# Kernel tuning notes

Measured on AMD Instinct MI355X. Metric: run time of the kernel, lower is better.

## Reference

```python
import jax, jax.numpy as jnp
import numpy as np

B_IMG, T_PER, DIN = 8, 4096, 1176
D, E, BN, L, TOP_K, OUT = 1024, 8, 64, 4, 2, 4096


def setup_inputs() -> dict:
    key = jax.random.key(0)
    ks = jax.random.split(key, 16)
    s = 0.02
    inp = {
        "pixel_values": jax.random.normal(ks[0], (B_IMG * T_PER, DIN), jnp.float32),
        "image_grid_thw": jnp.tile(jnp.array([[1, 64, 64]], dtype=jnp.int64), (B_IMG, 1)),
        # in_proj (no bias)
        "w_in": jax.random.normal(ks[1], (DIN, D), jnp.float32) * s,
        # skin classifier: Linear(D,64) -> ReLU -> Linear(64,3)
        "w_sc1": jax.random.normal(ks[2], (D, 64), jnp.float32) * s,
        "b_sc1": jnp.zeros((64,), jnp.float32),
        "w_sc2": jax.random.normal(ks[3], (64, 3), jnp.float32) * s,
        "b_sc2": jnp.zeros((3,), jnp.float32),
        # per-adapter-layer routers (stacked over L)
        "w_rimg": jax.random.normal(ks[4], (L, D, E), jnp.float32) * s,
        "w_rskin": jax.random.normal(ks[5], (L, 3, E), jnp.float32) * s,
        # per-layer, per-expert MLP: Linear(D,BN) -> ReLU -> Linear(BN,D)
        "ew1": jax.random.normal(ks[6], (L, E, D, BN), jnp.float32) * s,
        "eb1": jnp.zeros((L, E, BN), jnp.float32),
        "ew2": jax.random.normal(ks[7], (L, E, BN, D), jnp.float32) * s,
        "eb2": jnp.zeros((L, E, D), jnp.float32),
        # out_proj
        "w_out": jax.random.normal(ks[8], (D, OUT), jnp.float32) * s,
        "b_out": jnp.zeros((OUT,), jnp.float32),
    }
    return inp


def _forward(pixel_values, image_grid_thw, w_in, w_sc1, b_sc1, w_sc2, b_sc2,
             w_rimg, w_rskin, ew1, eb1, ew2, eb2, w_out, b_out):
    B = image_grid_thw.shape[0]
    T = pixel_values.shape[0] // B  # equal chunk sizes (t*h*w identical per image)
    x = pixel_values.reshape(B, T, -1)

    def per_image(xc):  # xc: [T, din]
        h = xc @ w_in  # [T, D]
        g = h.mean(0)
        skin_logits = jax.nn.relu(g @ w_sc1 + b_sc1) @ w_sc2 + b_sc2  # [3]
        skin_probs = jax.nn.softmax(skin_logits)

        def layer(carry, params):
            h, aux = carry
            wri, wrs, W1, B1, W2, B2 = params
            logits = h @ wri + skin_probs @ wrs  # [T, E]
            probs = jax.nn.softmax(logits, axis=-1)
            tp, ti = jax.lax.top_k(probs, TOP_K)
            tp = tp / (tp.sum(-1, keepdims=True) + 1e-6)
            rows = jnp.arange(h.shape[0])[:, None]
            # dense per-token expert weights (0 for non-selected experts)
            wfull = jnp.zeros_like(probs).at[rows, ti].add(tp)
            mask = jnp.zeros_like(probs).at[rows, ti].add(1.0)
            h1 = jax.nn.relu(jnp.einsum('td,edb->teb', h, W1) + B1)  # [T,E,BN]
            h2 = jnp.einsum('teb,ebd->ted', h1, W2) + B2             # [T,E,D]
            moe_out = jnp.einsum('ted,te->td', h2, wfull)
            aux = aux + (probs.mean(0) * mask.mean(0)).sum() * probs.shape[-1]
            return (h + moe_out, aux), None

        (h, aux), _ = jax.lax.scan(layer, (h, jnp.zeros((), h.dtype)),
                                   (w_rimg, w_rskin, ew1, eb1, ew2, eb2))
        return h.mean(0), skin_logits, aux

    pooled, skin_logits, aux = jax.vmap(per_image)(x)
    vision_proj = pooled @ w_out + b_out
    return pooled, vision_proj, aux.sum(), skin_logits


def reference(pixel_values, image_grid_thw, w_in, w_sc1, b_sc1, w_sc2, b_sc2,
              w_rimg, w_rskin, ew1, eb1, ew2, eb2, w_out, b_out):
    return _forward(pixel_values, image_grid_thw, w_in, w_sc1, b_sc1, w_sc2, b_sc2,
                    w_rimg, w_rskin, ew1, eb1, ew2, eb2, w_out, b_out)
```

## Files before the change

### kernel.cpp

```cpp
#include <hip/hip_runtime.h>
#include <math.h>

#define TPI  4096
#define TT   32768
#define DIN  1176
#define KP   1216
#define DM   1024
#define NE   8
#define BN   64
#define NL   4
#define DOUT 4096

typedef __attribute__((ext_vector_type(4))) float floatx4;
typedef __attribute__((ext_vector_type(8))) short bf16x8;
typedef unsigned int uint;

__device__ inline short f2bf(float x) {
    unsigned u = __float_as_uint(x);
    u += 0x7fffu + ((u >> 16) & 1u);
    return (short)(u >> 16);
}
__device__ inline float bf2f(short h) {
    return __uint_as_float(((unsigned)(unsigned short)h) << 16);
}

#define GLP(p) ((const __attribute__((address_space(1))) void*)(p))
#define LDSP(p) ((__attribute__((address_space(3))) void*)(p))
#define ASYNC16(g, s) __builtin_amdgcn_global_load_lds(GLP(g), LDSP(s), 16, 0, 0)

#define OFF_H0    0ul
#define OFF_H1    67108864ul
#define OFF_XB    67108864ul
#define OFF_WBT   146800640ul
#define OFF_E1T   149291008ul
#define OFF_E2T   153485312ul
#define OFF_BTOK  157679616ul
#define OFF_BW1   157810688ul
#define OFF_BW2   157941760ul
#define OFF_T2E   158072832ul
#define OFF_T2W   158203904ul
#define OFF_Z     158466048ul
#define Z_BYTES   39232ul
#define OFF_RB    158505280ul
#define OFF_WRT   158506304ul

__global__ __launch_bounds__(256) void convx_kernel(
    const float* __restrict__ X, short* __restrict__ Xb)
{
    const long row = blockIdx.x;
    const float* src = X + row * (long)DIN;
    short* dst = Xb + row * (long)KP;
    for (int i = threadIdx.x; i < 304; i += 256) {
        short4 s;
        if (i < 294) {
            float4 v = *(const float4*)(src + i * 4);
            s.x = f2bf(v.x); s.y = f2bf(v.y); s.z = f2bf(v.z); s.w = f2bf(v.w);
        } else {
            s.x = 0; s.y = 0; s.z = 0; s.w = 0;
        }
        *(short4*)(dst + i * 4) = s;
    }
}

__global__ __launch_bounds__(256) void transp_kernel(
    const float* __restrict__ src, short* __restrict__ dst, int RS, int CS, int DK)
{
    __shared__ float tb[64][65];
    const int kt = blockIdx.x * 64, nt = blockIdx.y * 64;
    const long sb = (long)blockIdx.z * RS * CS;
    const long db = (long)blockIdx.z * CS * DK;
    const int rr = threadIdx.x >> 6, cc = threadIdx.x & 63;
#pragma unroll
    for (int i = 0; i < 16; ++i) {
        int r = i * 4 + rr;
        int k = kt + r, n = nt + cc;
        tb[r][cc] = (k < RS && n < CS) ? src[sb + (long)k * CS + n] : 0.0f;
    }
    __syncthreads();
#pragma unroll
    for (int i = 0; i < 16; ++i) {
        int r = i * 4 + rr;
        int n = nt + r, k = kt + cc;
        if (n < CS && k < DK) dst[db + (long)n * DK + k] = f2bf(tb[cc][r]);
    }
}

__global__ __launch_bounds__(256) void wrt_kernel(
    const float* __restrict__ w_rimg, short* __restrict__ wrT)
{
    const int l = blockIdx.x >> 4, e = blockIdx.x & 15;
    short* dst = wrT + ((long)l * 16 + e) * 1024;
    if (e < 8) {
        const float* src = w_rimg + (long)l * 8192 + e;
        for (int k = threadIdx.x; k < 1024; k += 256) dst[k] = f2bf(src[k * 8]);
    } else {
        for (int k = threadIdx.x; k < 1024; k += 256) dst[k] = 0;
    }
}
// ... 7 lines not shown
    const int tid = threadIdx.x;
    const int m0 = blockIdx.x * 128, n0 = blockIdx.y * 128;
    const int w = tid >> 6, lane = tid & 63;
    const int quad = lane >> 4, l15 = lane & 15;
    const int wm = (w >> 1) * 64, wn = (w & 1) * 64;

    floatx4 acc[4][4];
#pragma unroll
    for (int i = 0; i < 4; ++i)
#pragma unroll
        for (int j = 0; j < 4; ++j) acc[i][j] = 0.0f;

    const int r = tid >> 3;
    const int gofs = ((tid & 7) ^ (r & 7)) * 8;
    const short* ap = Xb + (long)(m0 + r) * KP + gofs;
    const short* bp = Wbt + (long)(n0 + r) * KP + gofs;
    short* asd = As + tid * 8;
    short* bsd = Bs + tid * 8;
    const int rx = l15 & 7;

    for (int k0 = 0; k0 < KP; k0 += 64) {
        __syncthreads();
#pragma unroll
        for (int i = 0; i < 4; ++i) {
            ASYNC16(ap + (long)i * 32 * KP + k0, asd + i * 2048);
            ASYNC16(bp + (long)i * 32 * KP + k0, bsd + i * 2048);
        }
        __syncthreads();
#pragma unroll
        for (int kk = 0; kk < 2; ++kk) {
            bf16x8 af[4], bfr[4];
#pragma unroll
            for (int i = 0; i < 4; ++i)
                af[i] = *(const bf16x8*)&As[(wm + i * 16 + l15) * 64 + (((kk * 4 + quad)) ^ rx) * 8];
#pragma unroll
            for (int j = 0; j < 4; ++j)
                bfr[j] = *(const bf16x8*)&Bs[(wn + j * 16 + l15) * 64 + (((kk * 4 + quad)) ^ rx) * 8];
#pragma unroll
            for (int i = 0; i < 4; ++i)
#pragma unroll
                for (int j = 0; j < 4; ++j)
                    acc[i][j] = __builtin_amdgcn_mfma_f32_16x16x32_bf16(af[i], bfr[j], acc[i][j], 0, 0, 0);
        }
    }
    const int img = m0 >> 12;
#pragma unroll
    for (int j = 0; j < 4; ++j) {
        float cs = 0.0f;
#pragma unroll
        for (int i = 0; i < 4; ++i)
#pragma unroll
            for (int r2 = 0; r2 < 4; ++r2) {
                short hv = f2bf(acc[i][j][r2]);
                Hb[(long)(m0 + wm + i * 16 + quad * 4 + r2) * DM + n0 + wn + j * 16 + l15] = hv;
                cs += bf2f(hv);
            }
        cs += __shfl_xor(cs, 16);
        cs += __shfl_xor(cs, 32);
        if (quad == 0)
            atomicAdd(&g[img * DM + n0 + wn + j * 16 + l15], cs * (1.0f / 4096.0f));
    }
}

__global__ __launch_bounds__(256) void colmean_kernel(
    const short* __restrict__ Hb, float* __restrict__ outp)
{
    const int col = blockIdx.x * 256 + threadIdx.x;
    const int img = blockIdx.y;
    const int t0 = blockIdx.z * 256;
    const short* p = Hb + ((long)img * TPI + t0) * DM + col;
    float s = 0.0f;
#pragma unroll 8
    for (int t = 0; t < 256; ++t) s += bf2f(p[(long)t * DM]);
    atomicAdd(&outp[img * DM + col], s * (1.0f / 4096.0f));
}

__global__ __launch_bounds__(256) void skin1_kernel(
    const float* __restrict__ g, const float* __restrict__ w_sc1,
    const float* __restrict__ b_sc1, float* __restrict__ hsg)
{
    __shared__ float red[4][64];
    const int img = blockIdx.x;
    const int part = threadIdx.x >> 6, c = threadIdx.x & 63;
    float s = 0.0f;
    for (int i = 0; i < 256; ++i) {
        int d = part * 256 + i;
        s += g[img * DM + d] * w_sc1[d * 64 + c];
    }
    red[part][c] = s;
    __syncthreads();
    if (part == 0) {
        float v = red[0][c] + red[1][c] + red[2][c] + red[3][c] + b_sc1[c];
        hsg[img * 64 + c] = fmaxf(v, 0.0f);
    }
}

__global__ __launch_bounds__(256) void skin2_kernel(
    const float* __restrict__ hsg, const float* __restrict__ w_sc2, const float* __restrict__ b_sc2,
    const float* __restrict__ w_rskin, float* __restrict__ skin_logits_out, float* __restrict__ rb)
{
    __shared__ float l3[24];
    __shared__ float sp[24];
    const int tid = threadIdx.x;
    if (tid < 24) {
        int img = tid / 3, j = tid % 3;
        float s = b_sc2[j];
        for (int c = 0; c < 64; ++c) s += hsg[img * 64 + c] * w_sc2[c * 3 + j];
// ... 95 lines not shown
        }
#pragma unroll
        for (int e = 0; e < 8; ++e) {
            float rsum = p[e];
            for (int off = 32; off > 0; off >>= 1) rsum += __shfl_down(rsum, off);
            if (tid == 0) atomicAdd(&sum_probs[l * 64 + img * 8 + e], rsum);
        }
    }
}

__global__ __launch_bounds__(256) void scatter_kernel(
    const uint* __restrict__ top2e, const float* __restrict__ top2w,
    const int* __restrict__ counts_pair, int* __restrict__ cursors,
    int* __restrict__ btok, float* __restrict__ bw1, float* __restrict__ bw2, int l)
{
    __shared__ int pofS[64];
    const int tid = threadIdx.x;
    if (tid < 64) {
        int c = counts_pair[l * 64 + tid];
        int x = c;
#pragma unroll
        for (int off = 1; off < 64; off <<= 1) {
            int y = __shfl_up(x, off);
            if (tid >= off) x += y;
        }
        pofS[tid] = x - c;
    }
    __syncthreads();
    const int t = blockIdx.x * 256 + tid;
    const int lane = tid & 63;
    uint pe = top2e[t];
    int p = (int)(pe & 255u) * 8 + (int)((pe >> 8) & 255u);
    float w1 = top2w[2 * t], w2 = top2w[2 * t + 1];
    int myoff = pofS[p];
    unsigned long long rem = __ballot(true);
    while (rem) {
        int leader = __ffsll(rem) - 1;
        int pv = __shfl(p, leader);
        unsigned long long m = __ballot(p == pv);
        int basep = 0;
        if (lane == leader) basep = atomicAdd(&cursors[l * 64 + pv], __popcll(m));
        basep = __shfl(basep, leader);
        if (p == pv) {
            int pos = basep + __popcll(m & ((1ull << lane) - 1ull));
            int s = myoff + pos;
            btok[s] = t;
            bw1[s] = w1;
            bw2[s] = w2;
        }
        rem &= ~m;
    }
}

__global__ __launch_bounds__(256) void expert_pair(
    const short* __restrict__ Hin, short* __restrict__ Hout,
    int* __restrict__ counts_pair,
    const int* __restrict__ btok, const float* __restrict__ bw1, const float* __restrict__ bw2,
    const short* __restrict__ ew1t, const float* __restrict__ eb1,
    const short* __restrict__ ew2t, const float* __restrict__ eb2,
    const short* __restrict__ wrT, const float* __restrict__ rb,
    uint* __restrict__ top2e, float* __restrict__ top2w,
    float* __restrict__ sum_probs, float* __restrict__ mask_cnt, int l)
{
    __shared__ __align__(16) short As[8 * 64 * 32];
    __shared__ __align__(16) short h1a[64 * 72];
    __shared__ __align__(16) short h1b[64 * 72];
    __shared__ int tkS[64];
    __shared__ float w1S[64], w2S[64];
    __shared__ int pofS[64], cntS[64], tpS[64];
    __shared__ int nworkS;
    __shared__ float spLDS[64], mkLDS[64];

    const int tid = threadIdx.x;
    const int w = tid >> 6, lane = tid & 63;
    const int quad = lane >> 4, l15 = lane & 15;
    short* sdst = As + tid * 8;

    if (tid < 64) {
        int c = counts_pair[l * 64 + tid];
        cntS[tid] = c;
        int x = c;
#pragma unroll
        for (int off = 1; off < 64; off <<= 1) {
            int y = __shfl_up(x, off);
            if (tid >= off) x += y;
        }
        pofS[tid] = x - c;
        int nb = (c + 63) >> 6;
        int t = nb;
#pragma unroll
        for (int off = 1; off < 64; off <<= 1) {
            int y = __shfl_up(t, off);
            if (tid >= off) t += y;
        }
        tpS[tid] = t;
        if (tid == 63) nworkS = t;
    }
    __syncthreads();
    const int nwork = nworkS;

    for (int wi = blockIdx.x; wi < nwork; wi += gridDim.x) {
        int p = 0;
        while (p < 63 && tpS[p] <= wi) ++p;
        const int cnt = cntS[p];
        const int nbp = (cnt + 63) >> 6;
        const int base = (wi - (tpS[p] - nbp)) * 64;
        const int ea = p >> 3, eb = p & 7;
        const int off = pofS[p];

        __syncthreads();
        if (tid < 64) {
            bool valid = (base + tid) < cnt;
            int s = off + base + tid;
            tkS[tid] = valid ? btok[s] : 0;
            w1S[tid] = valid ? bw1[s] : 0.0f;
            w2S[tid] = valid ? bw2[s] : 0.0f;
            spLDS[tid] = 0.0f;
            mkLDS[tid] = 0.0f;
        }
        __syncthreads();
        const int lea = l * 8 + ea, leb = l * 8 + eb;
        const short* rowptr = Hin + (long)tkS[w * 16 + (lane >> 2)] * DM + (lane & 3) * 8;

        floatx4 acc1a[4], acc1b[4];
#pragma unroll
        for (int i = 0; i < 4; ++i) { acc1a[i] = 0.0f; acc1b[i] = 0.0f; }
        const short* w1ap = ew1t + ((long)lea * 64 + w * 16 + l15) * DM + quad * 8;
        const short* w1bp = ew1t + ((long)leb * 64 + w * 16 + l15) * DM + quad * 8;

        for (int k0 = 0; k0 < DM; k0 += 256) {
            __syncthreads();
#pragma unroll
            for (int c = 0; c < 8; ++c) ASYNC16(rowptr + k0 + c * 32, sdst + c * 2048);
            __syncthreads();
#pragma unroll
            for (int c = 0; c < 8; ++c) {
                bf16x8 ba = *(const bf16x8*)(w1ap + k0 + c * 32);
                bf16x8 bb = *(const bf16x8*)(w1bp + k0 + c * 32);
#pragma unroll
                for (int i = 0; i < 4; ++i) {
                    bf16x8 af = *(const bf16x8*)&As[c * 2048 + (i * 16 + l15) * 32 + quad * 8];
                    acc1a[i] = __builtin_amdgcn_mfma_f32_16x16x32_bf16(af, ba, acc1a[i], 0, 0, 0);
                    acc1b[i] = __builtin_amdgcn_mfma_f32_16x16x32_bf16(af, bb, acc1b[i], 0, 0, 0);
                }
            }
        }
        {
            float b1av = eb1[lea * BN + w * 16 + l15];
            float b1bv = eb1[leb * BN + w * 16 + l15];
#pragma unroll
            for (int i = 0; i < 4; ++i)
#pragma unroll
                for (int r = 0; r < 4; ++r) {
                    h1a[(i * 16 + quad * 4 + r) * 72 + w * 16 + l15] =
                        f2bf(fmaxf(acc1a[i][r] + b1av, 0.0f));
                    h1b[(i * 16 + quad * 4 + r) * 72 + w * 16 + l15] =
                        f2bf(fmaxf(acc1b[i][r] + b1bv, 0.0f));
                }
        }
        __syncthreads();

        const short* w2ap = ew2t + ((long)lea * DM + w * 16 + l15) * 64 + quad * 8;
        const short* w2bp = ew2t + ((long)leb * DM + w * 16 + l15) * 64 + quad * 8;
        const bool rowvalid = (base + (tid >> 2)) < cnt;
        const long orow = (long)tkS[tid >> 2] * DM;

        floatx4 acc_lg[4];
#pragma unroll
        for (int tf = 0; tf < 4; ++tf) acc_lg[tf] = 0.0f;

        for (int gidx = 0; gidx < 4; ++gidx) {
            const int g0 = gidx * 256;
#pragma unroll
            for (int c = 0; c < 8; ++c) ASYNC16(rowptr + g0 + c * 32, sdst + c * 2048);
            __syncthreads();
#pragma unroll
            for (int ns = 0; ns < 4; ++ns) {
                const int n0 = g0 + ns * 64;
                floatx4 a2a[4], a2b[4];
#pragma unroll
                for (int tj = 0; tj < 4; ++tj) { a2a[tj] = 0.0f; a2b[tj] = 0.0f; }
#pragma unroll
                for (int kk = 0; kk < 2; ++kk) {
                    bf16x8 wa = *(const bf16x8*)(w2ap + (long)n0 * 64 + kk * 32);
                    bf16x8 wb = *(const bf16x8*)(w2bp + (long)n0 * 64 + kk * 32);
#pragma unroll
                    for (int tj = 0; tj < 4; ++tj) {
                        bf16x8 ha = *(const bf16x8*)&h1a[(tj * 16 + l15) * 72 + kk * 32 + quad * 8];
                        bf16x8 hb = *(const bf16x8*)&h1b[(tj * 16 + l15) * 72 + kk * 32 + quad * 8];
                        a2a[tj] = __builtin_amdgcn_mfma_f32_16x16x32_bf16(wa, ha, a2a[tj], 0, 0, 0);
                        a2b[tj] = __builtin_amdgcn_mfma_f32_16x16x32_bf16(wb, hb, a2b[tj], 0, 0, 0);
                    }
                }
                const int nloc = ns * 64 + w * 16 + quad * 4;
                const int csub = nloc >> 5, cidx = nloc & 31;
                float4 b2av = *(const float4*)&eb2[lea * DM + g0 + nloc];
                float4 b2bv = *(const float4*)&eb2[leb * DM + g0 + nloc];
#pragma unroll
                for (int tj = 0; tj < 4; ++tj) {
                    int tk = tj * 16 + l15;
                    float w1 = w1S[tk], w2 = w2S[tk];
                    short* slot = &As[csub * 2048 + tk * 32 + cidx];
                    short4 res = *(short4*)slot;
                    short4 o;
                    o.x = f2bf(bf2f(res.x) + w1 * (a2a[tj][0] + b2av.x) + w2 * (a2b[tj][0] + b2bv.x));
                    o.y = f2bf(bf2f(res.y) + w1 * (a2a[tj][1] + b2av.y) + w2 * (a2b[tj][1] + b2bv.y));
                    o.z = f2bf(bf2f(res.z) + w1 * (a2a[tj][2] + b2av.z) + w2 * (a2b[tj][2] + b2bv.z));
                    o.w = f2bf(bf2f(res.w) + w1 * (a2a[tj][3] + b2av.w) + w2 * (a2b[tj][3] + b2bv.w));
                    *(short4*)slot = o;
                }
            }
            __syncthreads();

            if (l < 3) {
                const short* wrp = wrT + ((long)(l + 1) * 16 + l15) * 1024 + g0 + w * 64 + quad * 8;
#pragma unroll
                for (int kk = 0; kk < 2; ++kk) {
                    bf16x8 wf = *(const bf16x8*)(wrp + kk * 32);
#pragma unroll
                    for (int tf = 0; tf < 4; ++tf) {
                        bf16x8 of = *(const bf16x8*)&As[(w * 2 + kk) * 2048 + (tf * 16 + l15) * 32 + quad * 8];
                        acc_lg[tf] = __builtin_amdgcn_mfma_f32_16x16x32_bf16(wf, of, acc_lg[tf], 0, 0, 0);
                    }
                }
            }
            if (rowvalid) {
                const int tok = tid >> 2;
#pragma unroll
                for (int c2 = 0; c2 < 2; ++c2) {
                    const int csub = (tid & 3) * 2 + c2;
#pragma unroll
                    for (int j = 0; j < 4; ++j) {
                        int4 v = *(const int4*)&As[csub * 2048 + tok * 32 + j * 8];
                        *(int4*)(Hout + orow + g0 + csub * 32 + j * 8) = v;
                    }
                }
            }
            __syncthreads();
        }

        if (l < 3) {
            float* lgF = (float*)As;
#pragma unroll
            for (int tf = 0; tf < 4; ++tf)
                *(floatx4*)&lgF[(w * 64 + tf * 16 + l15) * 16 + quad * 4] = acc_lg[tf];
            __syncthreads();
            if (tid < 64) {
                const bool valid = (base + tid) < cnt;
                const int token = tkS[tid];
                const int img = token >> 12;
                float pb[8]; float mx = -1e30f;
#pragma unroll
                for (int e = 0; e < 8; ++e) {
                    float v = lgF[tid * 16 + e] + lgF[(64 + tid) * 16 + e]
                            + lgF[(128 + tid) * 16 + e] + lgF[(192 + tid) * 16 + e]
                            + rb[(l + 1) * 64 + img * 8 + e];
                    pb[e] = v; mx = fmaxf(mx, v);
                }
                float s = 0.0f;
#pragma unroll
                for (int e = 0; e < 8; ++e) { pb[e] = expf(pb[e] - mx); s += pb[e]; }
                float inv = 1.0f / s;
#pragma unroll
                for (int e = 0; e < 8; ++e) pb[e] *= inv;
                int i1 = 0; float b1v = pb[0];
#pragma unroll
                for (int e = 1; e < 8; ++e) if (pb[e] > b1v) { b1v = pb[e]; i1 = e; }
                int i2 = -1; float b2v = -1.0f;
#pragma unroll
                for (int e = 0; e < 8; ++e) if (e != i1 && pb[e] > b2v) { b2v = pb[e]; i2 = e; }
                if (valid) {
                    float den = b1v + b2v + 1e-6f;
                    top2e[token] = (uint)i1 | ((uint)i2 << 8);
                    top2w[2 * token] = b1v / den;
                    top2w[2 * token + 1] = b2v / den;
                    atomicAdd(&counts_pair[(l + 1) * 64 + i1 * 8 + i2], 1);
#pragma unroll
                    for (int e = 0; e < 8; ++e) atomicAdd(&spLDS[img * 8 + e], pb[e]);
                    atomicAdd(&mkLDS[img * 8 + i1], 1.0f);
                    atomicAdd(&mkLDS[img * 8 + i2], 1.0f);
                }
            }
            __syncthreads();
            if (tid < 64) {
                float v = spLDS[tid];
                if (v != 0.0f) atomicAdd(&sum_probs[(l + 1) * 64 + tid], v);
                float mz = mkLDS[tid];
                if (mz != 0.0f) atomicAdd(&mask_cnt[(l + 1) * 64 + tid], mz);
            }
        }
    }
}

__global__ __launch_bounds__(256) void vproj_kernel(
    const float* __restrict__ pooled, const float* __restrict__ w_out,
    const float* __restrict__ b_out, float* __restrict__ outp)
{
    __shared__ float ps[8 * 128];
    const int tid = threadIdx.x;
    const int n = blockIdx.x * 256 + tid;
    const int d0 = blockIdx.y * 128;
#pragma unroll
    for (int i = 0; i < 4; ++i) {
        int idx = tid + i * 256;
        ps[idx] = pooled[(idx >> 7) * DM + d0 + (idx & 127)];
    }
    __syncthreads();
    float acc[8];
    float binit = (blockIdx.y == 0) ? b_out[n] : 0.0f;
#pragma unroll
    for (int img = 0; img < 8; ++img) acc[img] = binit;
    for (int d = 0; d < 128; ++d) {
        float wv = w_out[(long)(d0 + d) * DOUT + n];
#pragma unroll
        for (int img = 0; img < 8; ++img) acc[img] += ps[img * 128 + d] * wv;
    }
#pragma unroll
    for (int img = 0; img < 8; ++img) atomicAdd(&outp[img * DOUT + n], acc[img]);
}

__global__ __launch_bounds__(64) void aux_kernel(
    const float* __restrict__ sum_probs, const float* __restrict__ mask_cnt,
    float* __restrict__ outp)
{
    const int tid = threadIdx.x;
    float v = 0.0f;
    if (tid < 32) {
        float s = 0.0f;
#pragma unroll
        for (int e = 0; e < 8; ++e) s += sum_probs[tid * 8 + e] * mask_cnt[tid * 8 + e];
        v = s * (8.0f / (4096.0f * 4096.0f));
    }
    for (int off = 32; off > 0; off >>= 1) v += __shfl_down(v, off);
    if (tid == 0) outp[0] = v;
}

extern "C" void kernel_launch(void* const* d_in, const int* in_sizes, int n_in,
                              void* d_out, int out_size, void* d_ws, size_t ws_size,
                              hipStream_t stream) {
    const float* X       = (const float*)d_in[0];
    const float* w_in    = (const float*)d_in[2];
    const float* w_sc1   = (const float*)d_in[3];
    const float* b_sc1   = (const float*)d_in[4];
    const float* w_sc2   = (const float*)d_in[5];
    const float* b_sc2   = (const float*)d_in[6];
    const float* w_rimg  = (const float*)d_in[7];
    const float* w_rskin = (const float*)d_in[8];
    const float* ew1     = (const float*)d_in[9];
    const float* eb1     = (const float*)d_in[10];
    const float* ew2     = (const float*)d_in[11];
    const float* eb2     = (const float*)d_in[12];
    const float* w_out   = (const float*)d_in[13];
    const float* b_out   = (const float*)d_in[14];

    float* out = (float*)d_out;
    char* ws = (char*)d_ws;

    short* H0   = (short*)(ws + OFF_H0);
    short* H1   = (short*)(ws + OFF_H1);
    short* Xb   = (short*)(ws + OFF_XB);
    short* Wbt  = (short*)(ws + OFF_WBT);
    short* ew1t = (short*)(ws + OFF_E1T);
    short* ew2t = (short*)(ws + OFF_E2T);
    int*   btok = (int*)(ws + OFF_BTOK);
    float* bw1  = (float*)(ws + OFF_BW1);
    float* bw2  = (float*)(ws + OFF_BW2);
    uint*  top2e = (uint*)(ws + OFF_T2E);
    float* top2w = (float*)(ws + OFF_T2W);
    int*   counts_pair = (int*)(ws + OFF_Z);
    int*   cursors     = (int*)(ws + OFF_Z + 1024);
    float* sum_probs   = (float*)(ws + OFF_Z + 2368);
    float* mask_cnt    = (float*)(ws + OFF_Z + 3392);
    float* g           = (float*)(ws + OFF_Z + 4416);
    float* hsg         = (float*)(ws + OFF_Z + 37184);
    float* rb          = (float*)(ws + OFF_RB);
    short* wrT         = (short*)(ws + OFF_WRT);

    hipMemsetAsync(d_out, 0, (size_t)out_size * sizeof(float), stream);
    hipMemsetAsync(ws + OFF_Z, 0, Z_BYTES, stream);

    dim3 b256(256);
    convx_kernel<<<TT, b256, 0, stream>>>(X, Xb);
    transp_kernel<<<dim3(19, 16, 1), b256, 0, stream>>>(w_in, Wbt, DIN, DM, KP);
    transp_kernel<<<dim3(16, 1, 32), b256, 0, stream>>>(ew1, ew1t, DM, BN, DM);
    transp_kernel<<<dim3(1, 16, 32), b256, 0, stream>>>(ew2, ew2t, BN, DM, BN);
    wrt_kernel<<<64, b256, 0, stream>>>(w_rimg, wrT);
    gemm_in_mfma<<<dim3(256, 8), b256, 0, stream>>>(Xb, Wbt, H0, g);
    skin1_kernel<<<8, b256, 0, stream>>>(g, w_sc1, b_sc1, hsg);
    skin2_kernel<<<1, b256, 0, stream>>>(hsg, w_sc2, b_sc2, w_rskin, out + 40961, rb);
    router_kernel<<<512, b256, 0, stream>>>(H0, wrT, rb, top2e, top2w,
                                            counts_pair, sum_probs, mask_cnt, 0);

    short* Hc = H0;
    short* Hn = H1;
    for (int l = 0; l < NL; ++l) {
        scatter_kernel<<<128, b256, 0, stream>>>(top2e, top2w, counts_pair, cursors,
                                                 btok, bw1, bw2, l);
        expert_pair<<<576, b256, 0, stream>>>(Hc, Hn, counts_pair, btok, bw1, bw2,
                                              ew1t, eb1, ew2t, eb2, wrT, rb,
                                              top2e, top2w, sum_probs, mask_cnt, l);
        short* tmp = Hc; Hc = Hn; Hn = tmp;
    }
    colmean_kernel<<<dim3(4, 8, 16), b256, 0, stream>>>(Hc, out);
    vproj_kernel<<<dim3(16, 8), b256, 0, stream>>>(out, w_out, b_out, out + 8192);
    aux_kernel<<<1, 64, 0, stream>>>(sum_probs, mask_cnt, out + 40960);
}
```

Measured before the change: 1.419 ms.

## Stage full 64-token hidden tile in LDS once per expert-pair work item

Measured after the change: 1.557 ms. 1.1x slower.

```diff
diff --git a/kernel.cpp b/kernel.cpp
--- a/kernel.cpp
+++ b/kernel.cpp
@@ -44,6 +44,21 @@
 #define OFF_RB    158505280ul
 #define OFF_WRT   158506304ul
 
+#define EPS_XS    0
+#define EPS_H1A   131072
+#define EPS_H1B   140288
+#define EPS_LGF   131072
+#define EPS_TK    149504
+#define EPS_W1    149760
+#define EPS_W2    150016
+#define EPS_CNT   150272
+#define EPS_POF   150528
+#define EPS_TP    150784
+#define EPS_SP    151040
+#define EPS_MK    151296
+#define EPS_NW    151552
+#define EP_SMEM   151616
+
 __global__ __launch_bounds__(256) void convx_kernel(
     const float* __restrict__ X, short* __restrict__ Xb)
 {
@@ -157,7 +172,8 @@
 #pragma unroll
             for (int r2 = 0; r2 < 4; ++r2) {
                 short hv = f2bf(acc[i][j][r2]);
-                Hb[(long)(m0 + wm + i * 16 + quad * 4 + r2) * DM + n0 + wn + j * 16 + l15] = hv;
+                Hb[(long)(m0 + wm + i * 16 + quad * 4 + r2) * DM + n0 + wn + j * 16 + l15] =
+                    hv;
                 cs += bf2f(hv);
             }
         cs += __shfl_xor(cs, 16);
@@ -359,7 +375,7 @@
     }
 }
 
-__global__ __launch_bounds__(256) void expert_pair(
+__global__ __launch_bounds__(256, 1) void expert_pair(
     const short* __restrict__ Hin, short* __restrict__ Hout,
     int* __restrict__ counts_pair,
     const int* __restrict__ btok, const float* __restrict__ bw1, const float* __restrict__ bw2,
@@ -369,19 +385,25 @@
     uint* __restrict__ top2e, float* __restrict__ top2w,
     float* __restrict__ sum_probs, float* __restrict__ mask_cnt, int l)
 {
-    __shared__ __align__(16) short As[8 * 64 * 32];
-    __shared__ __align__(16) short h1a[64 * 72];
-    __shared__ __align__(16) short h1b[64 * 72];
-    __shared__ int tkS[64];
-    __shared__ float w1S[64], w2S[64];
-    __shared__ int pofS[64], cntS[64], tpS[64];
-    __shared__ int nworkS;
-    __shared__ float spLDS[64], mkLDS[64];
+    extern __shared__ __align__(16) char smem[];
+    short* Xs   = (short*)(smem + EPS_XS);
+    short* h1a  = (short*)(smem + EPS_H1A);
+    short* h1b  = (short*)(smem + EPS_H1B);
+    float* lgF  = (float*)(smem + EPS_LGF);
+    int*   tkS  = (int*)(smem + EPS_TK);
+    float* w1S  = (float*)(smem + EPS_W1);
+    float* w2S  = (float*)(smem + EPS_W2);
+    int*   cntS = (int*)(smem + EPS_CNT);
+    int*   pofS = (int*)(smem + EPS_POF);
+    int*   tpS  = (int*)(smem + EPS_TP);
+    float* spLDS = (float*)(smem + EPS_SP);
+    float* mkLDS = (float*)(smem + EPS_MK);
+    int*   nworkS = (int*)(smem + EPS_NW);
 
     const int tid = threadIdx.x;
     const int w = tid >> 6, lane = tid & 63;
     const int quad = lane >> 4, l15 = lane & 15;
-    short* sdst = As + tid * 8;
+    const int rx = l15 & 7;
 
     if (tid < 64) {
         int c = counts_pair[l * 64 + tid];
@@ -401,10 +423,10 @@
             if (tid >= off) t += y;
         }
         tpS[tid] = t;
-        if (tid == 63) nworkS = t;
+        if (tid == 63) nworkS[0] = t;
     }
     __syncthreads();
-    const int nwork = nworkS;
+    const int nwork = nworkS[0];
 
     for (int wi = blockIdx.x; wi < nwork; wi += gridDim.x) {
         int p = 0;
@@ -414,6 +436,7 @@
         const int base = (wi - (tpS[p] - nbp)) * 64;
         const int ea = p >> 3, eb = p & 7;
         const int off = pofS[p];
+        const int lea = l * 8 + ea, leb = l * 8 + eb;
 
         __syncthreads();
         if (tid < 64) {
@@ -426,30 +449,35 @@
             mkLDS[tid] = 0.0f;
         }
         __syncthreads();
-        const int lea = l * 8 + ea, leb = l * 8 + eb;
-        const short* rowptr = Hin + (long)tkS[w * 16 + (lane >> 2)] * DM + (lane & 3) * 8;
-
-        floatx4 acc1a[4], acc1b[4];
-#pragma unroll
-        for (int i = 0; i < 4; ++i) { acc1a[i] = 0.0f; acc1b[i] = 0.0f; }
+
+        {
+            const int hb = tid >> 7;
+            const int lch = tid & 127;
+#pragma unroll
+            for (int i = 0; i < 32; ++i) {
+                const int row = i * 2 + hb;
+                const int tok = tkS[row];
+                const short* src = Hin + (long)tok * DM + ((lch ^ (row & 7)) << 3);
+                ASYNC16(src, Xs + (i * 256 + tid) * 8);
+            }
+        }
         const short* w1ap = ew1t + ((long)lea * 64 + w * 16 + l15) * DM + quad * 8;
         const short* w1bp = ew1t + ((long)leb * 64 + w * 16 + l15) * DM + quad * 8;
-
-        for (int k0 = 0; k0 < DM; k0 += 256) {
-            __syncthreads();
-#pragma unroll
-            for (int c = 0; c < 8; ++c) ASYNC16(rowptr + k0 + c * 32, sdst + c * 2048);
-            __syncthreads();
-#pragma unroll
-            for (int c = 0; c < 8; ++c) {
-                bf16x8 ba = *(const bf16x8*)(w1ap + k0 + c * 32);
-                bf16x8 bb = *(const bf16x8*)(w1bp + k0 + c * 32);
-#pragma unroll
-                for (int i = 0; i < 4; ++i) {
-                    bf16x8 af = *(const bf16x8*)&As[c * 2048 + (i * 16 + l15) * 32 + quad * 8];
-                    acc1a[i] = __builtin_amdgcn_mfma_f32_16x16x32_bf16(af, ba, acc1a[i], 0, 0, 0);
-                    acc1b[i] = __builtin_amdgcn_mfma_f32_16x16x32_bf16(af, bb, acc1b[i], 0, 0, 0);
-                }
+        __syncthreads();
+
+        floatx4 acc1a[4], acc1b[4];
+#pragma unroll
+        for (int i = 0; i < 4; ++i) { acc1a[i] = 0.0f; acc1b[i] = 0.0f; }
+#pragma unroll 8
+        for (int ks = 0; ks < 32; ++ks) {
+            bf16x8 ba = *(const bf16x8*)(w1ap + ks * 32);
+            bf16x8 bb = *(const bf16x8*)(w1bp + ks * 32);
+            const int cpos = ((ks * 4 + quad) ^ rx) * 8;
+#pragma unroll
+            for (int i = 0; i < 4; ++i) {
+                bf16x8 af = *(const bf16x8*)&Xs[(i * 16 + l15) * 1024 + cpos];
+                acc1a[i] = __builtin_amdgcn_mfma_f32_16x16x32_bf16(af, ba, acc1a[i], 0, 0, 0);
+                acc1b[i] = __builtin_amdgcn_mfma_f32_16x16x32_bf16(af, bb, acc1b[i], 0, 0, 0);
             }
         }
         {
@@ -467,87 +495,85 @@
         }
         __syncthreads();
 
+        bf16x8 hra[2][4], hrb[2][4];
+#pragma unroll
+        for (int kk = 0; kk < 2; ++kk)
+#pragma unroll
+            for (int tj = 0; tj < 4; ++tj) {
+                hra[kk][tj] = *(const bf16x8*)&h1a[(tj * 16 + l15) * 72 + kk * 32 + quad * 8];
+                hrb[kk][tj] = *(const bf16x8*)&h1b[(tj * 16 + l15) * 72 + kk * 32 + quad * 8];
+            }
+
         const short* w2ap = ew2t + ((long)lea * DM + w * 16 + l15) * 64 + quad * 8;
         const short* w2bp = ew2t + ((long)leb * DM + w * 16 + l15) * 64 + quad * 8;
-        const bool rowvalid = (base + (tid >> 2)) < cnt;
-        const long orow = (long)tkS[tid >> 2] * DM;
-
-        floatx4 acc_lg[4];
-#pragma unroll
-        for (int tf = 0; tf < 4; ++tf) acc_lg[tf] = 0.0f;
-
-        for (int gidx = 0; gidx < 4; ++gidx) {
-            const int g0 = gidx * 256;
-#pragma unroll
-            for (int c = 0; c < 8; ++c) ASYNC16(rowptr + g0 + c * 32, sdst + c * 2048);
-            __syncthreads();
-#pragma unroll
-            for (int ns = 0; ns < 4; ++ns) {
-                const int n0 = g0 + ns * 64;
-                floatx4 a2a[4], a2b[4];
-#pragma unroll
-                for (int tj = 0; tj < 4; ++tj) { a2a[tj] = 0.0f; a2b[tj] = 0.0f; }
-#pragma unroll
-                for (int kk = 0; kk < 2; ++kk) {
-                    bf16x8 wa = *(const bf16x8*)(w2ap + (long)n0 * 64 + kk * 32);
-                    bf16x8 wb = *(const bf16x8*)(w2bp + (long)n0 * 64 + kk * 32);
-#pragma unroll
-                    for (int tj = 0; tj < 4; ++tj) {
-                        bf16x8 ha = *(const bf16x8*)&h1a[(tj * 16 + l15) * 72 + kk * 32 + quad * 8];
-                        bf16x8 hb = *(const bf16x8*)&h1b[(tj * 16 + l15) * 72 + kk * 32 + quad * 8];
-                        a2a[tj] = __builtin_amdgcn_mfma_f32_16x16x32_bf16(wa, ha, a2a[tj], 0, 0, 0);
-                        a2b[tj] = __builtin_amdgcn_mfma_f32_16x16x32_bf16(wb, hb, a2b[tj], 0, 0, 0);
-                    }
+        const int nl = w * 16 + quad * 4;
+
+        for (int sl = 0; sl < 16; ++sl) {
+            const int n0 = sl * 64;
+            floatx4 a2a[4], a2b[4];
+#pragma unroll
+            for (int tj = 0; tj < 4; ++tj) { a2a[tj] = 0.0f; a2b[tj] = 0.0f; }
+#pragma unroll
+            for (int kk = 0; kk < 2; ++kk) {
+                bf16x8 wa = *(const bf16x8*)(w2ap + (long)n0 * 64 + kk * 32);
+                bf16x8 wb = *(const bf16x8*)(w2bp + (long)n0 * 64 + kk * 32);
+#pragma unroll
+                for (int tj = 0; tj < 4; ++tj) {
+                    a2a[tj] = __builtin_amdgcn_mfma_f32_16x16x32_bf16(wa, hra[kk][tj], a2a[tj], 0, 0, 0);
+                    a2b[tj] = __builtin_amdgcn_mfma_f32_16x16x32_bf16(wb, hrb[kk][tj], a2b[tj], 0, 0, 0);
                 }
-                const int nloc = ns * 64 + w * 16 + quad * 4;
-                const int csub = nloc >> 5, cidx = nloc & 31;
-                float4 b2av = *(const float4*)&eb2[lea * DM + g0 + nloc];
-                float4 b2bv = *(const float4*)&eb2[leb * DM + g0 + nloc];
-#pragma unroll
-                for (int tj = 0; tj < 4; ++tj) {
-                    int tk = tj * 16 + l15;
-                    float w1 = w1S[tk], w2 = w2S[tk];
-                    short* slot = &As[csub * 2048 + tk * 32 + cidx];
-                    short4 res = *(short4*)slot;
-                    short4 o;
-                    o.x = f2bf(bf2f(res.x) + w1 * (a2a[tj][0] + b2av.x) + w2 * (a2b[tj][0] + b2bv.x));
-                    o.y = f2bf(bf2f(res.y) + w1 * (a2a[tj][1] + b2av.y) + w2 * (a2b[tj][1] + b2bv.y));
-                    o.z = f2bf(bf2f(res.z) + w1 * (a2a[tj][2] + b2av.z) + w2 * (a2b[tj][2] + b2bv.z));
-                    o.w = f2bf(bf2f(res.w) + w1 * (a2a[tj][3] + b2av.w) + w2 * (a2b[tj][3] + b2bv.w));
-                    *(short4*)slot = o;
+            }
+            const int gcol = n0 + nl;
+            const int cpos2 = ((gcol >> 3) ^ rx) * 8 + (gcol & 7);
+            float4 b2av = *(const float4*)&eb2[lea * DM + gcol];
+            float4 b2bv = *(const float4*)&eb2[leb * DM + gcol];
+#pragma unroll
+            for (int tj = 0; tj < 4; ++tj) {
+                int tk = tj * 16 + l15;
+                float w1v = w1S[tk], w2v = w2S[tk];
+                short* slot = &Xs[tk * 1024 + cpos2];
+                short4 res = *(short4*)slot;
+                short4 o;
+                o.x = f2bf(bf2f(res.x) + w1v * (a2a[tj][0] + b2av.x) + w2v * (a2b[tj][0] + b2bv.x));
+                o.y = f2bf(bf2f(res.y) + w1v * (a2a[tj][1] + b2av.y) + w2v * (a2b[tj][1] + b2bv.y));
+                o.z = f2bf(bf2f(res.z) + w1v * (a2a[tj][2] + b2av.z) + w2v * (a2b[tj][2] + b2bv.z));
+                o.w = f2bf(bf2f(res.w) + w1v * (a2a[tj][3] + b2av.w) + w2v * (a2b[tj][3] + b2bv.w));
+                *(short4*)slot = o;
+            }
+        }
+        __syncthreads();
+
+        {
+            const int orowi = tid >> 2;
+            const bool rowvalid = (base + orowi) < cnt;
+            if (rowvalid) {
+                const long orow = (long)tkS[orowi] * DM;
+                const int k = orowi & 7;
+#pragma unroll
+                for (int i = 0; i < 32; ++i) {
+                    const int ch = (tid & 3) + i * 4;
+                    int4 v = *(const int4*)&Xs[orowi * 1024 + ((ch ^ k) << 3)];
+                    *(int4*)(Hout + orow + (ch << 3)) = v;
                 }
             }
-            __syncthreads();
-
-            if (l < 3) {
-                const short* wrp = wrT + ((long)(l + 1) * 16 + l15) * 1024 + g0 + w * 64 + quad * 8;
-#pragma unroll
-                for (int kk = 0; kk < 2; ++kk) {
-                    bf16x8 wf = *(const bf16x8*)(wrp + kk * 32);
-#pragma unroll
-                    for (int tf = 0; tf < 4; ++tf) {
-                        bf16x8 of = *(const bf16x8*)&As[(w * 2 + kk) * 2048 + (tf * 16 + l15) * 32 + quad * 8];
-                        acc_lg[tf] = __builtin_amdgcn_mfma_f32_16x16x32_bf16(wf, of, acc_lg[tf], 0, 0, 0);
-                    }
+        }
+
+        if (l < 3) {
+            const short* wrp = wrT + ((long)(l + 1) * 16 + l15) * 1024 + quad * 8;
+            floatx4 acc_lg[4];
+#pragma unroll
+            for (int tf = 0; tf < 4; ++tf) acc_lg[tf] = 0.0f;
+#pragma unroll
+            for (int kl = 0; kl < 8; ++kl) {
+                const int ks = w * 8 + kl;
+                bf16x8 wf = *(const bf16x8*)(wrp + ks * 32);
+                const int cpos = ((ks * 4 + quad) ^ rx) * 8;
+#pragma unroll
+                for (int tf = 0; tf < 4; ++tf) {
+                    bf16x8 of = *(const bf16x8*)&Xs[(tf * 16 + l15) * 1024 + cpos];
+                    acc_lg[tf] = __builtin_amdgcn_mfma_f32_16x16x32_bf16(wf, of, acc_lg[tf], 0, 0, 0);
                 }
             }
-            if (rowvalid) {
-                const int tok = tid >> 2;
-#pragma unroll
-                for (int c2 = 0; c2 < 2; ++c2) {
-                    const int csub = (tid & 3) * 2 + c2;
-#pragma unroll
-                    for (int j = 0; j < 4; ++j) {
-                        int4 v = *(const int4*)&As[csub * 2048 + tok * 32 + j * 8];
-                        *(int4*)(Hout + orow + g0 + csub * 32 + j * 8) = v;
-                    }
-                }
-            }
-            __syncthreads();
-        }
-
-        if (l < 3) {
-            float* lgF = (float*)As;
 #pragma unroll
             for (int tf = 0; tf < 4; ++tf)
                 *(floatx4*)&lgF[(w * 64 + tf * 16 + l15) * 16 + quad * 4] = acc_lg[tf];
@@ -683,6 +709,13 @@
     float* rb          = (float*)(ws + OFF_RB);
     short* wrT         = (short*)(ws + OFF_WRT);
 
+    static bool attr_set = false;
+    if (!attr_set) {
+        hipFuncSetAttribute(reinterpret_cast<const void*>(expert_pair),
+                            hipFuncAttributeMaxDynamicSharedMemorySize, EP_SMEM);
+        attr_set = true;
+    }
+
     hipMemsetAsync(d_out, 0, (size_t)out_size * sizeof(float), stream);
     hipMemsetAsync(ws + OFF_Z, 0, Z_BYTES, stream);
 
@@ -703,9 +736,9 @@
     for (int l = 0; l < NL; ++l) {
         scatter_kernel<<<128, b256, 0, stream>>>(top2e, top2w, counts_pair, cursors,
                                                  btok, bw1, bw2, l);
-        expert_pair<<<576, b256, 0, stream>>>(Hc, Hn, counts_pair, btok, bw1, bw2,
-                                              ew1t, eb1, ew2t, eb2, wrT, rb,
-                                              top2e, top2w, sum_probs, mask_cnt, l);
+        expert_pair<<<576, b256, EP_SMEM, stream>>>(Hc, Hn, counts_pair, btok, bw1, bw2,
+                                                    ew1t, eb1, ew2t, eb2, wrT, rb,
+                                                    top2e, top2w, sum_probs, mask_cnt, l);
         short* tmp = Hc; Hc = Hn; Hn = tmp;
     }
     colmean_kernel<<<dim3(4, 8, 16), b256, 0, stream>>>(Hc, out);
```

## Restructure expert_pair into independent per-wave 16-token tiles without block barriers

Applied to the files above, without the earlier changes.

Measured after the change: 4.626 ms. 226% more time.

```diff
diff --git a/kernel.cpp b/kernel.cpp
--- a/kernel.cpp
+++ b/kernel.cpp
@@ -157,7 +157,8 @@
 #pragma unroll
             for (int r2 = 0; r2 < 4; ++r2) {
                 short hv = f2bf(acc[i][j][r2]);
-                Hb[(long)(m0 + wm + i * 16 + quad * 4 + r2) * DM + n0 + wn + j * 16 + l15] = hv;
+                Hb[(long)(m0 + wm + i * 16 + quad * 4 + r2) * DM + n0 + wn + j * 16 + l15] =
+                    hv;
                 cs += bf2f(hv);
             }
         cs += __shfl_xor(cs, 16);
@@ -359,7 +360,7 @@
     }
 }
 
-__global__ __launch_bounds__(256) void expert_pair(
+__global__ __launch_bounds__(256, 2) void expert_pair(
     const short* __restrict__ Hin, short* __restrict__ Hout,
     int* __restrict__ counts_pair,
     const int* __restrict__ btok, const float* __restrict__ bw1, const float* __restrict__ bw2,
@@ -369,231 +370,177 @@
     uint* __restrict__ top2e, float* __restrict__ top2w,
     float* __restrict__ sum_probs, float* __restrict__ mask_cnt, int l)
 {
-    __shared__ __align__(16) short As[8 * 64 * 32];
-    __shared__ __align__(16) short h1a[64 * 72];
-    __shared__ __align__(16) short h1b[64 * 72];
-    __shared__ int tkS[64];
-    __shared__ float w1S[64], w2S[64];
-    __shared__ int pofS[64], cntS[64], tpS[64];
-    __shared__ int nworkS;
-    __shared__ float spLDS[64], mkLDS[64];
+    __shared__ __align__(16) short h1aS[4][16 * 72];
+    __shared__ __align__(16) short h1bS[4][16 * 72];
+    __shared__ float lgWS[4][16 * 9];
 
     const int tid = threadIdx.x;
     const int w = tid >> 6, lane = tid & 63;
     const int quad = lane >> 4, l15 = lane & 15;
-    short* sdst = As + tid * 8;
-
-    if (tid < 64) {
-        int c = counts_pair[l * 64 + tid];
-        cntS[tid] = c;
-        int x = c;
-#pragma unroll
-        for (int off = 1; off < 64; off <<= 1) {
-            int y = __shfl_up(x, off);
-            if (tid >= off) x += y;
-        }
-        pofS[tid] = x - c;
-        int nb = (c + 63) >> 6;
-        int t = nb;
-#pragma unroll
-        for (int off = 1; off < 64; off <<= 1) {
-            int y = __shfl_up(t, off);
-            if (tid >= off) t += y;
-        }
-        tpS[tid] = t;
-        if (tid == 63) nworkS = t;
-    }
-    __syncthreads();
-    const int nwork = nworkS;
+    short* h1a = &h1aS[w][0];
+    short* h1b = &h1bS[w][0];
+    float* lgW = &lgWS[w][0];
+
+    int c = counts_pair[l * 64 + lane];
+    int x = c;
+#pragma unroll
+    for (int off = 1; off < 64; off <<= 1) {
+        int y = __shfl_up(x, off);
+        if (lane >= off) x += y;
+    }
+    const int pof = x - c;
+    int nb = (c + 63) >> 6;
+    int tp = nb;
+#pragma unroll
+    for (int off = 1; off < 64; off <<= 1) {
+        int y = __shfl_up(tp, off);
+        if (lane >= off) tp += y;
+    }
+    const int nwork = __shfl(tp, 63);
 
     for (int wi = blockIdx.x; wi < nwork; wi += gridDim.x) {
-        int p = 0;
-        while (p < 63 && tpS[p] <= wi) ++p;
-        const int cnt = cntS[p];
+        unsigned long long m = __ballot(tp > wi);
+        const int p = (int)(__ffsll(m) - 1);
+        const int cnt = __shfl(c, p);
+        const int tstart = __shfl(pof, p);
+        const int tp_p = __shfl(tp, p);
         const int nbp = (cnt + 63) >> 6;
-        const int base = (wi - (tpS[p] - nbp)) * 64;
+        const int base64 = (wi - (tp_p - nbp)) * 64;
+        const int sbase = base64 + w * 16;
+        if (sbase >= cnt) continue;
+
         const int ea = p >> 3, eb = p & 7;
-        const int off = pofS[p];
-
-        __syncthreads();
-        if (tid < 64) {
-            bool valid = (base + tid) < cnt;
-            int s = off + base + tid;
-            tkS[tid] = valid ? btok[s] : 0;
-            w1S[tid] = valid ? bw1[s] : 0.0f;
-            w2S[tid] = valid ? bw2[s] : 0.0f;
-            spLDS[tid] = 0.0f;
-            mkLDS[tid] = 0.0f;
-        }
-        __syncthreads();
         const int lea = l * 8 + ea, leb = l * 8 + eb;
-        const short* rowptr = Hin + (long)tkS[w * 16 + (lane >> 2)] * DM + (lane & 3) * 8;
-
-        floatx4 acc1a[4], acc1b[4];
-#pragma unroll
-        for (int i = 0; i < 4; ++i) { acc1a[i] = 0.0f; acc1b[i] = 0.0f; }
-        const short* w1ap = ew1t + ((long)lea * 64 + w * 16 + l15) * DM + quad * 8;
-        const short* w1bp = ew1t + ((long)leb * 64 + w * 16 + l15) * DM + quad * 8;
-
-        for (int k0 = 0; k0 < DM; k0 += 256) {
-            __syncthreads();
-#pragma unroll
-            for (int c = 0; c < 8; ++c) ASYNC16(rowptr + k0 + c * 32, sdst + c * 2048);
-            __syncthreads();
-#pragma unroll
-            for (int c = 0; c < 8; ++c) {
-                bf16x8 ba = *(const bf16x8*)(w1ap + k0 + c * 32);
-                bf16x8 bb = *(const bf16x8*)(w1bp + k0 + c * 32);
-#pragma unroll
-                for (int i = 0; i < 4; ++i) {
-                    bf16x8 af = *(const bf16x8*)&As[c * 2048 + (i * 16 + l15) * 32 + quad * 8];
-                    acc1a[i] = __builtin_amdgcn_mfma_f32_16x16x32_bf16(af, ba, acc1a[i], 0, 0, 0);
-                    acc1b[i] = __builtin_amdgcn_mfma_f32_16x16x32_bf16(af, bb, acc1b[i], 0, 0, 0);
+
+        const int slot = sbase + l15;
+        const bool valid = slot < cnt;
+        const int gidx = tstart + (valid ? slot : 0);
+        const int tok = valid ? btok[gidx] : 0;
+        const float wv1 = valid ? bw1[gidx] : 0.0f;
+        const float wv2 = valid ? bw2[gidx] : 0.0f;
+
+        const short* tA  = Hin + (long)tok * DM + quad * 8;
+        const short* w1a = ew1t + ((long)lea * BN + l15) * DM + quad * 8;
+        const short* w1b = ew1t + ((long)leb * BN + l15) * DM + quad * 8;
+
+        floatx4 a1a[4], a1b[4];
+#pragma unroll
+        for (int nf = 0; nf < 4; ++nf) { a1a[nf] = 0.0f; a1b[nf] = 0.0f; }
+#pragma unroll
+        for (int ks = 0; ks < 32; ++ks) {
+            bf16x8 af = *(const bf16x8*)(tA + ks * 32);
+#pragma unroll
+            for (int nf = 0; nf < 4; ++nf) {
+                bf16x8 ba = *(const bf16x8*)(w1a + (long)nf * 16 * DM + ks * 32);
+                bf16x8 bb = *(const bf16x8*)(w1b + (long)nf * 16 * DM + ks * 32);
+                a1a[nf] = __builtin_amdgcn_mfma_f32_16x16x32_bf16(af, ba, a1a[nf], 0, 0, 0);
+                a1b[nf] = __builtin_amdgcn_mfma_f32_16x16x32_bf16(af, bb, a1b[nf], 0, 0, 0);
+            }
+        }
+#pragma unroll
+        for (int nf = 0; nf < 4; ++nf) {
+            float b1av = eb1[lea * BN + nf * 16 + l15];
+            float b1bv = eb1[leb * BN + nf * 16 + l15];
+#pragma unroll
+            for (int r = 0; r < 4; ++r) {
+                h1a[(quad * 4 + r) * 72 + nf * 16 + l15] =
+                    f2bf(fmaxf(a1a[nf][r] + b1av, 0.0f));
+                h1b[(quad * 4 + r) * 72 + nf * 16 + l15] =
+                    f2bf(fmaxf(a1b[nf][r] + b1bv, 0.0f));
+            }
+        }
+        bf16x8 ha[2], hb[2];
+#pragma unroll
+        for (int kk = 0; kk < 2; ++kk) {
+            ha[kk] = *(const bf16x8*)&h1a[l15 * 72 + kk * 32 + quad * 8];
+            hb[kk] = *(const bf16x8*)&h1b[l15 * 72 + kk * 32 + quad * 8];
+        }
+
+        const short* w2a = ew2t + ((long)lea * DM + l15) * 64 + quad * 8;
+        const short* w2b = ew2t + ((long)leb * DM + l15) * 64 + quad * 8;
+        const short* wrp = (l < 3) ? (wrT + ((long)(l + 1) * 16 + l15) * 1024 + quad * 8)
+                                   : wrT;
+        const short* resp = Hin + (long)tok * DM;
+        short* outp = Hout + (long)tok * DM;
+
+        floatx4 accR = 0.0f;
+#pragma unroll
+        for (int ks = 0; ks < 32; ++ks) {
+            int2 opair[2];
+#pragma unroll
+            for (int s = 0; s < 2; ++s) {
+                const int nf = 2 * ks + s;
+                floatx4 a2a = 0.0f, a2b = 0.0f;
+#pragma unroll
+                for (int kk = 0; kk < 2; ++kk) {
+                    bf16x8 wa = *(const bf16x8*)(w2a + (long)nf * 1024 + kk * 32);
+                    bf16x8 wb = *(const bf16x8*)(w2b + (long)nf * 1024 + kk * 32);
+                    a2a = __builtin_amdgcn_mfma_f32_16x16x32_bf16(wa, ha[kk], a2a, 0, 0, 0);
+                    a2b = __builtin_amdgcn_mfma_f32_16x16x32_bf16(wb, hb[kk], a2b, 0, 0, 0);
                 }
-            }
-        }
-        {
-            float b1av = eb1[lea * BN + w * 16 + l15];
-            float b1bv = eb1[leb * BN + w * 16 + l15];
-#pragma unroll
-            for (int i = 0; i < 4; ++i)
-#pragma unroll
-                for (int r = 0; r < 4; ++r) {
-                    h1a[(i * 16 + quad * 4 + r) * 72 + w * 16 + l15] =
-                        f2bf(fmaxf(acc1a[i][r] + b1av, 0.0f));
-                    h1b[(i * 16 + quad * 4 + r) * 72 + w * 16 + l15] =
-                        f2bf(fmaxf(acc1b[i][r] + b1bv, 0.0f));
+                const int ncol = nf * 16 + quad * 4;
+                float4 b2av = *(const float4*)&eb2[lea * DM + ncol];
+                float4 b2bv = *(const float4*)&eb2[leb * DM + ncol];
+                short4 res = *(const short4*)(resp + ncol);
+                short4 o;
+                o.x = f2bf(bf2f(res.x) + wv1 * (a2a[0] + b2av.x) + wv2 * (a2b[0] + b2bv.x));
+                o.y = f2bf(bf2f(res.y) + wv1 * (a2a[1] + b2av.y) + wv2 * (a2b[1] + b2bv.y));
+                o.z = f2bf(bf2f(res.z) + wv1 * (a2a[2] + b2av.z) + wv2 * (a2b[2] + b2bv.z));
+                o.w = f2bf(bf2f(res.w) + wv1 * (a2a[3] + b2av.w) + wv2 * (a2b[3] + b2bv.w));
+                if (valid) *(short4*)(outp + ncol) = o;
+                union { short4 s4; int2 i2v; } pu; pu.s4 = o; opair[s] = pu.i2v;
+            }
+            if (l < 3) {
+                int sx = (quad & 2) ? opair[1].x : opair[0].x;
+                int sy = (quad & 2) ? opair[1].y : opair[0].y;
+                int slo = l15 + ((quad & 1) << 5);
+                int shi = slo + 16;
+                int4 ai;
+                ai.x = __shfl(sx, slo); ai.y = __shfl(sy, slo);
+                ai.z = __shfl(sx, shi); ai.w = __shfl(sy, shi);
+                union { int4 i4; bf16x8 v; } au; au.i4 = ai;
+                bf16x8 wrB = *(const bf16x8*)(wrp + ks * 32);
+                accR = __builtin_amdgcn_mfma_f32_16x16x32_bf16(au.v, wrB, accR, 0, 0, 0);
+            }
+        }
+
+        if (l < 3) {
+            if (l15 < 8) {
+#pragma unroll
+                for (int r = 0; r < 4; ++r) lgW[(quad * 4 + r) * 9 + l15] = accR[r];
+            }
+            if (lane < 16) {
+                if (valid) {
+                    const int img = tok >> 12;
+                    float pb[8]; float mx = -1e30f;
+#pragma unroll
+                    for (int e = 0; e < 8; ++e) {
+                        float v = lgW[lane * 9 + e] + rb[(l + 1) * 64 + img * 8 + e];
+                        pb[e] = v; mx = fmaxf(mx, v);
+                    }
+                    float s = 0.0f;
+#pragma unroll
+                    for (int e = 0; e < 8; ++e) { pb[e] = expf(pb[e] - mx); s += pb[e]; }
+                    float inv = 1.0f / s;
+#pragma unroll
+                    for (int e = 0; e < 8; ++e) pb[e] *= inv;
+                    int i1 = 0; float b1v = pb[0];
+#pragma unroll
+                    for (int e = 1; e < 8; ++e) if (pb[e] > b1v) { b1v = pb[e]; i1 = e; }
+                    int i2 = -1; float b2v = -1.0f;
+#pragma unroll
+                    for (int e = 0; e < 8; ++e) if (e != i1 && pb[e] > b2v) { b2v = pb[e]; i2 = e; }
+                    float den = b1v + b2v + 1e-6f;
+                    top2e[tok] = (uint)i1 | ((uint)i2 << 8);
+                    top2w[2 * tok] = b1v / den;
+                    top2w[2 * tok + 1] = b2v / den;
+                    atomicAdd(&counts_pair[(l + 1) * 64 + i1 * 8 + i2], 1);
+#pragma unroll
+                    for (int e = 0; e < 8; ++e)
+                        atomicAdd(&sum_probs[(l + 1) * 64 + img * 8 + e], pb[e]);
+                    atomicAdd(&mask_cnt[(l + 1) * 64 + img * 8 + i1], 1.0f);
+                    atomicAdd(&mask_cnt[(l + 1) * 64 + img * 8 + i2], 1.0f);
                 }
-        }
-        __syncthreads();
-
-        const short* w2ap = ew2t + ((long)lea * DM + w * 16 + l15) * 64 + quad * 8;
-        const short* w2bp = ew2t + ((long)leb * DM + w * 16 + l15) * 64 + quad * 8;
-        const bool rowvalid = (base + (tid >> 2)) < cnt;
-        const long orow = (long)tkS[tid >> 2] * DM;
-
-        floatx4 acc_lg[4];
-#pragma unroll
-        for (int tf = 0; tf < 4; ++tf) acc_lg[tf] = 0.0f;
-
-        for (int gidx = 0; gidx < 4; ++gidx) {
-            const int g0 = gidx * 256;
-#pragma unroll
-            for (int c = 0; c < 8; ++c) ASYNC16(rowptr + g0 + c * 32, sdst + c * 2048);
-            __syncthreads();
-#pragma unroll
-            for (int ns = 0; ns < 4; ++ns) {
-                const int n0 = g0 + ns * 64;
-                floatx4 a2a[4], a2b[4];
-#pragma unroll
-                for (int tj = 0; tj < 4; ++tj) { a2a[tj] = 0.0f; a2b[tj] = 0.0f; }
-#pragma unroll
-                for (int kk = 0; kk < 2; ++kk) {
-                    bf16x8 wa = *(const bf16x8*)(w2ap + (long)n0 * 64 + kk * 32);
-                    bf16x8 wb = *(const bf16x8*)(w2bp + (long)n0 * 64 + kk * 32);
-#pragma unroll
-                    for (int tj = 0; tj < 4; ++tj) {
-                        bf16x8 ha = *(const bf16x8*)&h1a[(tj * 16 + l15) * 72 + kk * 32 + quad * 8];
-                        bf16x8 hb = *(const bf16x8*)&h1b[(tj * 16 + l15) * 72 + kk * 32 + quad * 8];
-                        a2a[tj] = __builtin_amdgcn_mfma_f32_16x16x32_bf16(wa, ha, a2a[tj], 0, 0, 0);
-                        a2b[tj] = __builtin_amdgcn_mfma_f32_16x16x32_bf16(wb, hb, a2b[tj], 0, 0, 0);
-                    }
-                }
-                const int nloc = ns * 64 + w * 16 + quad * 4;
-                const int csub = nloc >> 5, cidx = nloc & 31;
-                float4 b2av = *(const float4*)&eb2[lea * DM + g0 + nloc];
-                float4 b2bv = *(const float4*)&eb2[leb * DM + g0 + nloc];
-#pragma unroll
-                for (int tj = 0; tj < 4; ++tj) {
-                    int tk = tj * 16 + l15;
-                    float w1 = w1S[tk], w2 = w2S[tk];
-                    short* slot = &As[csub * 2048 + tk * 32 + cidx];
-                    short4 res = *(short4*)slot;
-                    short4 o;
-                    o.x = f2bf(bf2f(res.x) + w1 * (a2a[tj][0] + b2av.x) + w2 * (a2b[tj][0] + b2bv.x));
-                    o.y = f2bf(bf2f(res.y) + w1 * (a2a[tj][1] + b2av.y) + w2 * (a2b[tj][1] + b2bv.y));
-                    o.z = f2bf(bf2f(res.z) + w1 * (a2a[tj][2] + b2av.z) + w2 * (a2b[tj][2] + b2bv.z));
-                    o.w = f2bf(bf2f(res.w) + w1 * (a2a[tj][3] + b2av.w) + w2 * (a2b[tj][3] + b2bv.w));
-                    *(short4*)slot = o;
-                }
-            }
-            __syncthreads();
-
-            if (l < 3) {
-                const short* wrp = wrT + ((long)(l + 1) * 16 + l15) * 1024 + g0 + w * 64 + quad * 8;
-#pragma unroll
-                for (int kk = 0; kk < 2; ++kk) {
-                    bf16x8 wf = *(const bf16x8*)(wrp + kk * 32);
-#pragma unroll
-                    for (int tf = 0; tf < 4; ++tf) {
-                        bf16x8 of = *(const bf16x8*)&As[(w * 2 + kk) * 2048 + (tf * 16 + l15) * 32 + quad * 8];
-                        acc_lg[tf] = __builtin_amdgcn_mfma_f32_16x16x32_bf16(wf, of, acc_lg[tf], 0, 0, 0);
-                    }
-                }
-            }
-            if (rowvalid) {
-                const int tok = tid >> 2;
-#pragma unroll
-                for (int c2 = 0; c2 < 2; ++c2) {
-                    const int csub = (tid & 3) * 2 + c2;
-#pragma unroll
-                    for (int j = 0; j < 4; ++j) {
-                        int4 v = *(const int4*)&As[csub * 2048 + tok * 32 + j * 8];
-                        *(int4*)(Hout + orow + g0 + csub * 32 + j * 8) = v;
-                    }
-                }
-            }
-            __syncthreads();
-        }
-
-        if (l < 3) {
-            float* lgF = (float*)As;
-#pragma unroll
-            for (int tf = 0; tf < 4; ++tf)
-                *(floatx4*)&lgF[(w * 64 + tf * 16 + l15) * 16 + quad * 4] = acc_lg[tf];
-            __syncthreads();
-            if (tid < 64) {
-                const bool valid = (base + tid) < cnt;
-                const int token = tkS[tid];
-                const int img = token >> 12;
-                float pb[8]; float mx = -1e30f;
-#pragma unroll
-                for (int e = 0; e < 8; ++e) {
-                    float v = lgF[tid * 16 + e] + lgF[(64 + tid) * 16 + e]
-                            + lgF[(128 + tid) * 16 + e] + lgF[(192 + tid) * 16 + e]
-                            + rb[(l + 1) * 64 + img * 8 + e];
-                    pb[e] = v; mx = fmaxf(mx, v);
-                }
-                float s = 0.0f;
-#pragma unroll
-                for (int e = 0; e < 8; ++e) { pb[e] = expf(pb[e] - mx); s += pb[e]; }
-                float inv = 1.0f / s;
-#pragma unroll
-                for (int e = 0; e < 8; ++e) pb[e] *= inv;
-                int i1 = 0; float b1v = pb[0];
-#pragma unroll
-                for (int e = 1; e < 8; ++e) if (pb[e] > b1v) { b1v = pb[e]; i1 = e; }
-                int i2 = -1; float b2v = -1.0f;
-#pragma unroll
-                for (int e = 0; e < 8; ++e) if (e != i1 && pb[e] > b2v) { b2v = pb[e]; i2 = e; }
-                if (valid) {
-                    float den = b1v + b2v + 1e-6f;
-                    top2e[token] = (uint)i1 | ((uint)i2 << 8);
-                    top2w[2 * token] = b1v / den;
-                    top2w[2 * token + 1] = b2v / den;
-                    atomicAdd(&counts_pair[(l + 1) * 64 + i1 * 8 + i2], 1);
-#pragma unroll
-                    for (int e = 0; e < 8; ++e) atomicAdd(&spLDS[img * 8 + e], pb[e]);
-                    atomicAdd(&mkLDS[img * 8 + i1], 1.0f);
-                    atomicAdd(&mkLDS[img * 8 + i2], 1.0f);
-                }
-            }
-            __syncthreads();
-            if (tid < 64) {
-                float v = spLDS[tid];
-                if (v != 0.0f) atomicAdd(&sum_probs[(l + 1) * 64 + tid], v);
-                float mz = mkLDS[tid];
-                if (mz != 0.0f) atomicAdd(&mask_cnt[(l + 1) * 64 + tid], mz);
             }
         }
     }
```
